# Optimization experiments

Measured on AMD Instinct MI355X. Metric: run time of the kernel, lower is better.

## Reference

```python
import jax, jax.numpy as jnp
import numpy as np

N_NODES = 256
DIM = 128
N_LAYERS = 3
LN_EPS = 1e-5


def setup_inputs() -> dict:
    key = jax.random.key(0)
    ks = jax.random.split(key, 8)
    B = 2048
    node_features = jax.random.normal(ks[0], (B, N_NODES, DIM), dtype=jnp.float32)
    A_logits_pos = jax.random.normal(ks[1], (N_NODES, N_NODES), dtype=jnp.float32) * 0.01
    A_logits_neg = jax.random.normal(ks[2], (N_NODES, N_NODES), dtype=jnp.float32) * 0.01
    # per-layer Linear weights, torch layout (out_dim, in_dim); all dims are 128
    scale = 1.0 / np.sqrt(DIM)
    W_pos = jax.random.uniform(ks[3], (N_LAYERS, DIM, DIM), jnp.float32, -scale, scale)
    W_neg = jax.random.uniform(ks[4], (N_LAYERS, DIM, DIM), jnp.float32, -scale, scale)
    ln_g = jnp.ones((N_LAYERS, DIM), jnp.float32)
    ln_b = jnp.zeros((N_LAYERS, DIM), jnp.float32)
    ro_g = jnp.ones((DIM,), jnp.float32)
    ro_b = jnp.zeros((DIM,), jnp.float32)
    return {"node_features": node_features, "A_logits_pos": A_logits_pos,
            "A_logits_neg": A_logits_neg, "W_pos": W_pos, "W_neg": W_neg,
            "ln_g": ln_g, "ln_b": ln_b, "ro_g": ro_g, "ro_b": ro_b}


def _layernorm(x, g, b):
    mu = jnp.mean(x, axis=-1, keepdims=True)
    var = jnp.var(x, axis=-1, keepdims=True)
    return (x - mu) * jax.lax.rsqrt(var + LN_EPS) * g + b


def reference(node_features, A_logits_pos, A_logits_neg, W_pos, W_neg, ln_g, ln_b, ro_g, ro_b):
    # soft signed adjacency with hard-mask split (mask is non-differentiable)
    A_p = jax.nn.sigmoid(A_logits_pos)
    A_n = jax.nn.sigmoid(A_logits_neg)
    mask = (A_p > A_n).astype(A_p.dtype)
    A_pos = A_p * mask
    A_neg = A_n * (1.0 - mask)

    H = node_features  # (B, N, D)
    for l in range(N_LAYERS):
        agg_pos = jnp.einsum('uv,bvd->bud', A_pos, H)
        agg_neg = jnp.einsum('uv,bvd->bud', A_neg, H)
        # torch Linear: x @ W.T ; GELU is exact (erf) by default in torch
        out = jax.nn.gelu(jnp.einsum('bud,od->buo', agg_pos, W_pos[l])
                          - jnp.einsum('bud,od->buo', agg_neg, W_neg[l]),
                          approximate=False)
        H = _layernorm(out, ln_g[l], ln_b[l])  # dropout = identity in eval

    h_G = jnp.mean(H, axis=1)  # (B, D) readout
    return _layernorm(h_G, ro_g, ro_b)
```

## Files before the change

### kernel.cpp

```cpp
#include <hip/hip_runtime.h>
#include <math.h>


typedef float  f32x4  __attribute__((ext_vector_type(4)));
typedef float  f32x16 __attribute__((ext_vector_type(16)));
typedef short  s16x8  __attribute__((ext_vector_type(8)));
typedef __bf16 bf16x8 __attribute__((ext_vector_type(8)));

#define GOFF 65536

__device__ __forceinline__ unsigned short f2bf(float f) {
  __bf16 h = (__bf16)f;
  return __builtin_bit_cast(unsigned short, h);
}
__device__ __forceinline__ float bf2f(unsigned short h) {
  return __builtin_bit_cast(float, (unsigned int)h << 16);
}
__device__ __forceinline__ unsigned short f2bf_rne(float f) {
  unsigned int u = __builtin_bit_cast(unsigned int, f);
  u = (u + 0x7fffu + ((u >> 16) & 1u)) >> 16;
  return (unsigned short)u;
}

__device__ __forceinline__ int haddr(int v, int d) {
  return v * 256 + ((d * 2) ^ ((v & 15) << 4));
}
__device__ __forceinline__ int gaddr(int o, int vr) {
  return GOFF + o * 80 + vr * 2;
}

#define MFMA32(a, b, c) __builtin_amdgcn_mfma_f32_32x32x16_bf16( \
    __builtin_bit_cast(bf16x8, (a)), __builtin_bit_cast(bf16x8, (b)), (c), 0, 0, 0)

__global__ void prep_kernel(const float* __restrict__ alp, const float* __restrict__ aln,
                            const float* __restrict__ wp,  const float* __restrict__ wn,
                            unsigned short* __restrict__ A3, unsigned short* __restrict__ W3) {
  int idx = blockIdx.x * 512 + threadIdx.x;
  if (idx < 131072) {
    int j = idx & 7, lane = (idx >> 3) & 63, vt = (idx >> 9) & 15,
        ut = (idx >> 13) & 7, h = (idx >> 16) & 1;
    int u = ut * 32 + (lane & 31);
    int v = vt * 16 + (lane >> 5) * 8 + j;
    int s = u * 256 + v;
    float ap = 1.f / (1.f + expf(-alp[s]));
    float an = 1.f / (1.f + expf(-aln[s]));
    bool  m  = ap > an;
    float val = h ? (m ? 0.f : -an) : (m ? ap : 0.f);
    A3[idx] = f2bf_rne(val);
  } else {
    int k = idx - 131072;
    int j = k & 7, lane = (k >> 3) & 63, kt = (k >> 9) & 7,
        ot = (k >> 12) & 3, hw = (k >> 14);
    int o = ot * 32 + (lane & 31);
    int d = kt * 16 + (lane >> 5) * 8 + j;
    const float* src = (hw & 1) ? wn : wp;
    W3[k] = f2bf_rne(src[(hw >> 1) * 16384 + o * 128 + d]);
  }
}

__global__ __launch_bounds__(256, 2) void gnn_kernel(
    const float* __restrict__ X,
    const unsigned short* __restrict__ A3,
    const unsigned short* __restrict__ W3,
    const float* __restrict__ ln_g, const float* __restrict__ ln_b,
    const float* __restrict__ ro_g, const float* __restrict__ ro_b,
    float* __restrict__ out) {
  extern __shared__ char smem[];
  const int tid  = threadIdx.x;
  const int wid  = tid >> 6;
  const int lane = tid & 63;
  const int l31  = lane & 31;
  const int hi   = lane >> 5;
  const int b    = blockIdx.x;

  {
    const float4* Xb = (const float4*)(X + (size_t)b * 256 * 128);
#pragma unroll 8
    for (int i = 0; i < 32; ++i) {
      int idx = tid + i * 256;
      int v = idx >> 5, d = (idx & 31) * 4;
      float4 f = Xb[idx];
      ushort4 p;
      p.x = f2bf(f.x); p.y = f2bf(f.y); p.z = f2bf(f.z); p.w = f2bf(f.w);
      *(ushort4*)(smem + haddr(v, d)) = p;
    }
  }
  __syncthreads();

  f32x16 acc[2][4];
  for (int l = 0; l < 3; ++l) {
#pragma unroll
    for (int mt = 0; mt < 2; ++mt)
#pragma unroll
      for (int nt = 0; nt < 4; ++nt)
#pragma unroll
        for (int r = 0; r < 16; ++r) acc[mt][nt][r] = 0.f;

    for (int h = 0; h < 2; ++h) {
      const unsigned short* Wb = W3 + (size_t)(((l * 2 + h) * 4 + wid) * 8) * 512;
      const unsigned short* Ab = A3 + (size_t)((h * 8 + wid * 2) * 16) * 512;

      s16x8 wreg[8];
#pragma unroll
      for (int kt = 0; kt < 8; ++kt)
        wreg[kt] = *(const s16x8*)(Wb + (size_t)kt * 512 + lane * 8);

      for (int c = 0; c < 8; ++c) {
        s16x8 pa[4];
#pragma unroll
        for (int kt = 0; kt < 2; ++kt) {
          pa[kt * 2 + 0] = *(const s16x8*)(Ab + (size_t)(0 * 16 + c * 2 + kt) * 512 + lane * 8);
          pa[kt * 2 + 1] = *(const s16x8*)(Ab + (size_t)(1 * 16 + c * 2 + kt) * 512 + lane * 8);
        }

        f32x16 g0;
#pragma unroll
        for (int r = 0; r < 16; ++r) g0[r] = 0.f;
        const int v0 = c * 32 + l31;
#pragma unroll
        for (int kt = 0; kt < 8; ++kt) {
          s16x8 ha = *(const s16x8*)(smem + haddr(v0, kt * 16 + hi * 8));
          g0 = MFMA32(ha, wreg[kt], g0);
        }
        __syncthreads();
        {
          const int og = wid * 32 + l31;
#pragma unroll
          for (int rq = 0; rq < 4; ++rq) {
            int vr = rq * 8 + hi * 4;
            ushort4 p;
            p.x = f2bf(g0[rq*4+0]); p.y = f2bf(g0[rq*4+1]);
            p.z = f2bf(g0[rq*4+2]); p.w = f2bf(g0[rq*4+3]);
            *(ushort4*)(smem + gaddr(og, vr)) = p;
          }
        }
        __syncthreads();

#pragma unroll
        for (int kt = 0; kt < 2; ++kt) {
#pragma unroll
          for (int nt = 0; nt < 4; ++nt) {
            s16x8 bf = *(const s16x8*)(smem + gaddr(nt * 32 + l31, kt * 16 + hi * 8));
            acc[0][nt] = MFMA32(pa[kt * 2 + 0], bf, acc[0][nt]);
            acc[1][nt] = MFMA32(pa[kt * 2 + 1], bf, acc[1][nt]);
          }
        }
      }
    }

    {
      float lg[4], lb[4];
#pragma unroll
      for (int nt = 0; nt < 4; ++nt) {
        lg[nt] = ln_g[l * 128 + nt * 32 + l31];
        lb[nt] = ln_b[l * 128 + nt * 32 + l31];
      }
#pragma unroll
      for (int mt = 0; mt < 2; ++mt)
#pragma unroll
        for (int r = 0; r < 16; ++r) {
          float x0 = acc[mt][0][r]; x0 = 0.5f * x0 * (1.f + erff(x0 * 0.70710678f));
          float x1 = acc[mt][1][r]; x1 = 0.5f * x1 * (1.f + erff(x1 * 0.70710678f));
          float x2 = acc[mt][2][r]; x2 = 0.5f * x2 * (1.f + erff(x2 * 0.70710678f));
          float x3 = acc[mt][3][r]; x3 = 0.5f * x3 * (1.f + erff(x3 * 0.70710678f));
          acc[mt][0][r] = x0; acc[mt][1][r] = x1;
          acc[mt][2][r] = x2; acc[mt][3][r] = x3;
          float s1 = x0 + x1 + x2 + x3;
          float s2 = x0 * x0 + x1 * x1 + x2 * x2 + x3 * x3;
#pragma unroll
          for (int m = 1; m < 32; m <<= 1) {
            s1 += __shfl_xor(s1, m);
            s2 += __shfl_xor(s2, m);
          }
          float mu  = s1 * (1.f / 128.f);
          float var = s2 * (1.f / 128.f) - mu * mu;
          float rs  = rsqrtf(var + 1e-5f);
          int u = wid * 64 + mt * 32 + (r & 3) + 8 * ((r >> 2) & 3) + 4 * hi;
#pragma unroll
          for (int nt = 0; nt < 4; ++nt) {
            float y = (acc[mt][nt][r] - mu) * rs * lg[nt] + lb[nt];
            *(unsigned short*)(smem + haddr(u, nt * 32 + l31)) = f2bf(y);
          }
        }
    }
    __syncthreads();
  }

  {
    int d   = tid & 127;
    int grp = tid >> 7;
    float s = 0.f;
    for (int v = grp * 128; v < grp * 128 + 128; ++v)
      s += bf2f(*(const unsigned short*)(smem + haddr(v, d)));
    float* red = (float*)(smem + GOFF);
    red[grp * 128 + d] = s;
    __syncthreads();
    if (tid < 128) {
      red[256 + tid] = (red[tid] + red[128 + tid]) * (1.f / 256.f);
    }
    __syncthreads();
    if (tid < 64) {
      float a  = red[256 + tid];
      float b2 = red[256 + 64 + tid];
      float s1 = a + b2, s2 = a * a + b2 * b2;
#pragma unroll
      for (int m = 1; m < 64; m <<= 1) {
        s1 += __shfl_xor(s1, m);
        s2 += __shfl_xor(s2, m);
      }
      float mu  = s1 * (1.f / 128.f);
      float var = s2 * (1.f / 128.f) - mu * mu;
      float rs  = rsqrtf(var + 1e-5f);
      out[(size_t)b * 128 + tid]      = (a  - mu) * rs * ro_g[tid]      + ro_b[tid];
      out[(size_t)b * 128 + 64 + tid] = (b2 - mu) * rs * ro_g[64 + tid] + ro_b[64 + tid];
    }
  }
}

extern "C" void kernel_launch(void* const* d_in, const int* in_sizes, int n_in,
                              void* d_out, int out_size, void* d_ws, size_t ws_size,
                              hipStream_t stream) {
  const float* X   = (const float*)d_in[0];
  const float* alp = (const float*)d_in[1];
  const float* aln = (const float*)d_in[2];
  const float* wp  = (const float*)d_in[3];
  const float* wn  = (const float*)d_in[4];
  const float* lng = (const float*)d_in[5];
  const float* lnb = (const float*)d_in[6];
  const float* rog = (const float*)d_in[7];
  const float* rob = (const float*)d_in[8];
  float* out = (float*)d_out;

  unsigned short* A3 = (unsigned short*)d_ws;
  unsigned short* W3 = A3 + 131072;

  (void)hipFuncSetAttribute(reinterpret_cast<const void*>(gnn_kernel),
                            hipFuncAttributeMaxDynamicSharedMemorySize, 75776);

  prep_kernel<<<448, 512, 0, stream>>>(alp, aln, wp, wn, A3, W3);
  gnn_kernel<<<2048, 256, 75776, stream>>>(X, A3, W3, lng, lnb, rog, rob, out);
}
```

Before: 654.0 us.

## Merge positive and negative branches per chunk to halve block barriers

Instead of two separate passes for the positive and negative adjacency halves, each 32-row chunk now computes both H·Wp and H·Wn projections and stages them side by side in shared memory as a 64-wide K slice. The A matmul then runs K=64 per chunk, so the number of __syncthreads pairs per layer drops from 16 to 8. The G staging buffer uses an XOR-swizzled 128-byte row layout to avoid bank conflicts. In exchange, negative weights are reloaded from global memory on every chunk instead of being held in registers, and shared memory per block grows to 81920 bytes, which may reduce occupancy.

```diff
diff --git a/kernel.cpp b/kernel.cpp
--- a/kernel.cpp
+++ b/kernel.cpp
@@ -25,8 +25,8 @@
 __device__ __forceinline__ int haddr(int v, int d) {
   return v * 256 + ((d * 2) ^ ((v & 15) << 4));
 }
-__device__ __forceinline__ int gaddr(int o, int vr) {
-  return GOFF + o * 80 + vr * 2;
+__device__ __forceinline__ int gaddr(int o, int k) {
+  return GOFF + o * 128 + ((k * 2) ^ ((o & 7) << 4));
 }
 
 #define MFMA32(a, b, c) __builtin_amdgcn_mfma_f32_32x32x16_bf16( \
@@ -96,54 +96,56 @@
 #pragma unroll
         for (int r = 0; r < 16; ++r) acc[mt][nt][r] = 0.f;
 
-    for (int h = 0; h < 2; ++h) {
-      const unsigned short* Wb = W3 + (size_t)(((l * 2 + h) * 4 + wid) * 8) * 512;
-      const unsigned short* Ab = A3 + (size_t)((h * 8 + wid * 2) * 16) * 512;
-
-      s16x8 wreg[8];
-#pragma unroll
-      for (int kt = 0; kt < 8; ++kt)
-        wreg[kt] = *(const s16x8*)(Wb + (size_t)kt * 512 + lane * 8);
-
-      for (int c = 0; c < 8; ++c) {
-        s16x8 pa[4];
-#pragma unroll
-        for (int kt = 0; kt < 2; ++kt) {
-          pa[kt * 2 + 0] = *(const s16x8*)(Ab + (size_t)(0 * 16 + c * 2 + kt) * 512 + lane * 8);
-          pa[kt * 2 + 1] = *(const s16x8*)(Ab + (size_t)(1 * 16 + c * 2 + kt) * 512 + lane * 8);
+    const unsigned short* WbP = W3 + (size_t)(((l * 2 + 0) * 4 + wid) * 8) * 512;
+    const unsigned short* WbN = W3 + (size_t)(((l * 2 + 1) * 4 + wid) * 8) * 512;
+
+    s16x8 wregP[8];
+#pragma unroll
+    for (int kt = 0; kt < 8; ++kt)
+      wregP[kt] = *(const s16x8*)(WbP + (size_t)kt * 512 + lane * 8);
+
+    for (int c = 0; c < 8; ++c) {
+      f32x16 g0, g1;
+#pragma unroll
+      for (int r = 0; r < 16; ++r) { g0[r] = 0.f; g1[r] = 0.f; }
+      const int v0 = c * 32 + l31;
+#pragma unroll
+      for (int kt = 0; kt < 8; ++kt) {
+        s16x8 ha = *(const s16x8*)(smem + haddr(v0, kt * 16 + hi * 8));
+        s16x8 wn = *(const s16x8*)(WbN + (size_t)kt * 512 + lane * 8);
+        g0 = MFMA32(ha, wregP[kt], g0);
+        g1 = MFMA32(ha, wn, g1);
+      }
+      __syncthreads();
+      {
+        const int og = wid * 32 + l31;
+#pragma unroll
+        for (int rq = 0; rq < 4; ++rq) {
+          int kr = rq * 8 + hi * 4;
+          ushort4 p;
+          p.x = f2bf(g0[rq*4+0]); p.y = f2bf(g0[rq*4+1]);
+          p.z = f2bf(g0[rq*4+2]); p.w = f2bf(g0[rq*4+3]);
+          *(ushort4*)(smem + gaddr(og, kr)) = p;
+          p.x = f2bf(g1[rq*4+0]); p.y = f2bf(g1[rq*4+1]);
+          p.z = f2bf(g1[rq*4+2]); p.w = f2bf(g1[rq*4+3]);
+          *(ushort4*)(smem + gaddr(og, 32 + kr)) = p;
         }
-
-        f32x16 g0;
-#pragma unroll
-        for (int r = 0; r < 16; ++r) g0[r] = 0.f;
-        const int v0 = c * 32 + l31;
-#pragma unroll
-        for (int kt = 0; kt < 8; ++kt) {
-          s16x8 ha = *(const s16x8*)(smem + haddr(v0, kt * 16 + hi * 8));
-          g0 = MFMA32(ha, wreg[kt], g0);
-        }
-        __syncthreads();
-        {
-          const int og = wid * 32 + l31;
-#pragma unroll
-          for (int rq = 0; rq < 4; ++rq) {
-            int vr = rq * 8 + hi * 4;
-            ushort4 p;
-            p.x = f2bf(g0[rq*4+0]); p.y = f2bf(g0[rq*4+1]);
-            p.z = f2bf(g0[rq*4+2]); p.w = f2bf(g0[rq*4+3]);
-            *(ushort4*)(smem + gaddr(og, vr)) = p;
-          }
-        }
-        __syncthreads();
-
-#pragma unroll
-        for (int kt = 0; kt < 2; ++kt) {
-#pragma unroll
-          for (int nt = 0; nt < 4; ++nt) {
-            s16x8 bf = *(const s16x8*)(smem + gaddr(nt * 32 + l31, kt * 16 + hi * 8));
-            acc[0][nt] = MFMA32(pa[kt * 2 + 0], bf, acc[0][nt]);
-            acc[1][nt] = MFMA32(pa[kt * 2 + 1], bf, acc[1][nt]);
-          }
+      }
+      __syncthreads();
+
+#pragma unroll
+      for (int kt = 0; kt < 4; ++kt) {
+        const int h   = kt >> 1;
+        const int vtk = c * 2 + (kt & 1);
+        const unsigned short* Ab =
+            A3 + (size_t)(((h * 8 + wid * 2) * 16 + vtk)) * 512;
+        s16x8 a0 = *(const s16x8*)(Ab + lane * 8);
+        s16x8 a1 = *(const s16x8*)(Ab + 16 * 512 + lane * 8);
+#pragma unroll
+        for (int nt = 0; nt < 4; ++nt) {
+          s16x8 bf = *(const s16x8*)(smem + gaddr(nt * 32 + l31, kt * 16 + hi * 8));
+          acc[0][nt] = MFMA32(a0, bf, acc[0][nt]);
+          acc[1][nt] = MFMA32(a1, bf, acc[1][nt]);
         }
       }
     }
@@ -235,8 +237,8 @@
   unsigned short* W3 = A3 + 131072;
 
   (void)hipFuncSetAttribute(reinterpret_cast<const void*>(gnn_kernel),
-                            hipFuncAttributeMaxDynamicSharedMemorySize, 75776);
+                            hipFuncAttributeMaxDynamicSharedMemorySize, 81920);
 
   prep_kernel<<<448, 512, 0, stream>>>(alp, aln, wp, wn, A3, W3);
-  gnn_kernel<<<2048, 256, 75776, stream>>>(X, A3, W3, lng, lnb, rog, rob, out);
-}
+  gnn_kernel<<<2048, 256, 81920, stream>>>(X, A3, W3, lng, lnb, rog, rob, out);
+}
```

Result: slower. 763.2 us (+16.7%).

## Process 64-node chunks per iteration and XOR-swizzle the G staging buffer

Applied to the files above, without the earlier changes.

Doubles the v-chunk processed per loop iteration from 32 to 64 nodes. This halves the number of chunk iterations and their pairs of __syncthreads, and issues two independent MFMA chains in the H·W stage. The G staging buffer is widened to 64 columns with an XOR swizzle instead of padding, meant to keep LDS accesses free of bank conflicts. The A fragments are now loaded inside the K loop instead of being preloaded. LDS use grows to 80KB per block, which should still allow 2 blocks per CU on a 160KB LDS.

```diff
diff --git a/kernel.cpp b/kernel.cpp
--- a/kernel.cpp
+++ b/kernel.cpp
@@ -25,8 +25,8 @@
 __device__ __forceinline__ int haddr(int v, int d) {
   return v * 256 + ((d * 2) ^ ((v & 15) << 4));
 }
-__device__ __forceinline__ int gaddr(int o, int vr) {
-  return GOFF + o * 80 + vr * 2;
+__device__ __forceinline__ int gaddr(int o, int v) {
+  return GOFF + o * 128 + ((v * 2) ^ ((o & 7) << 4));
 }
 
 #define MFMA32(a, b, c) __builtin_amdgcn_mfma_f32_32x32x16_bf16( \
@@ -105,22 +105,18 @@
       for (int kt = 0; kt < 8; ++kt)
         wreg[kt] = *(const s16x8*)(Wb + (size_t)kt * 512 + lane * 8);
 
-      for (int c = 0; c < 8; ++c) {
-        s16x8 pa[4];
-#pragma unroll
-        for (int kt = 0; kt < 2; ++kt) {
-          pa[kt * 2 + 0] = *(const s16x8*)(Ab + (size_t)(0 * 16 + c * 2 + kt) * 512 + lane * 8);
-          pa[kt * 2 + 1] = *(const s16x8*)(Ab + (size_t)(1 * 16 + c * 2 + kt) * 512 + lane * 8);
-        }
-
-        f32x16 g0;
-#pragma unroll
-        for (int r = 0; r < 16; ++r) g0[r] = 0.f;
-        const int v0 = c * 32 + l31;
+      for (int c = 0; c < 4; ++c) {
+        f32x16 ga, gb;
+#pragma unroll
+        for (int r = 0; r < 16; ++r) { ga[r] = 0.f; gb[r] = 0.f; }
+        const int va = c * 64 + l31;
+        const int vb = va + 32;
 #pragma unroll
         for (int kt = 0; kt < 8; ++kt) {
-          s16x8 ha = *(const s16x8*)(smem + haddr(v0, kt * 16 + hi * 8));
-          g0 = MFMA32(ha, wreg[kt], g0);
+          s16x8 h0 = *(const s16x8*)(smem + haddr(va, kt * 16 + hi * 8));
+          s16x8 h1 = *(const s16x8*)(smem + haddr(vb, kt * 16 + hi * 8));
+          ga = MFMA32(h0, wreg[kt], ga);
+          gb = MFMA32(h1, wreg[kt], gb);
         }
         __syncthreads();
         {
@@ -129,20 +125,25 @@
           for (int rq = 0; rq < 4; ++rq) {
             int vr = rq * 8 + hi * 4;
             ushort4 p;
-            p.x = f2bf(g0[rq*4+0]); p.y = f2bf(g0[rq*4+1]);
-            p.z = f2bf(g0[rq*4+2]); p.w = f2bf(g0[rq*4+3]);
+            p.x = f2bf(ga[rq*4+0]); p.y = f2bf(ga[rq*4+1]);
+            p.z = f2bf(ga[rq*4+2]); p.w = f2bf(ga[rq*4+3]);
             *(ushort4*)(smem + gaddr(og, vr)) = p;
+            p.x = f2bf(gb[rq*4+0]); p.y = f2bf(gb[rq*4+1]);
+            p.z = f2bf(gb[rq*4+2]); p.w = f2bf(gb[rq*4+3]);
+            *(ushort4*)(smem + gaddr(og, 32 + vr)) = p;
           }
         }
         __syncthreads();
 
 #pragma unroll
-        for (int kt = 0; kt < 2; ++kt) {
+        for (int kt = 0; kt < 4; ++kt) {
+          s16x8 a0 = *(const s16x8*)(Ab + (size_t)(0 * 16 + c * 4 + kt) * 512 + lane * 8);
+          s16x8 a1 = *(const s16x8*)(Ab + (size_t)(1 * 16 + c * 4 + kt) * 512 + lane * 8);
 #pragma unroll
           for (int nt = 0; nt < 4; ++nt) {
             s16x8 bf = *(const s16x8*)(smem + gaddr(nt * 32 + l31, kt * 16 + hi * 8));
-            acc[0][nt] = MFMA32(pa[kt * 2 + 0], bf, acc[0][nt]);
-            acc[1][nt] = MFMA32(pa[kt * 2 + 1], bf, acc[1][nt]);
+            acc[0][nt] = MFMA32(a0, bf, acc[0][nt]);
+            acc[1][nt] = MFMA32(a1, bf, acc[1][nt]);
           }
         }
       }
@@ -235,8 +236,8 @@
   unsigned short* W3 = A3 + 131072;
 
   (void)hipFuncSetAttribute(reinterpret_cast<const void*>(gnn_kernel),
-                            hipFuncAttributeMaxDynamicSharedMemorySize, 75776);
+                            hipFuncAttributeMaxDynamicSharedMemorySize, 81920);
 
   prep_kernel<<<448, 512, 0, stream>>>(alp, aln, wp, wn, A3, W3);
-  gnn_kernel<<<2048, 256, 75776, stream>>>(X, A3, W3, lng, lnb, rog, rob, out);
-}
+  gnn_kernel<<<2048, 256, 81920, stream>>>(X, A3, W3, lng, lnb, rog, rob, out);
+}
```

Result: slower. 1.052 ms (+60.9%).
